# Kernel optimization log

Hardware: AMD Instinct MI355X
Metric: run time of the kernel (lower is better)

Reference implementation:

```python
import jax, jax.numpy as jnp
import numpy as np

B, S, H, I, G = 4, 2048, 2048, 8192, 128


def _onebit_quant(w, group_size):
    # Group-wise 1-bit (sign) quantization along the input dim with per-group
    # abs-mean scale, as in BitNet-style OneBitLinear.
    out_f, in_f = w.shape
    wg = w.reshape(out_f, in_f // group_size, group_size)
    scale = jnp.mean(jnp.abs(wg), axis=-1, keepdims=True)  # [out, n_groups, 1]
    wq = jnp.sign(wg) * scale
    return wq.reshape(out_f, in_f)


def setup_inputs() -> dict:
    key = jax.random.key(0)
    k1, k2, k3, k4 = jax.random.split(key, 4)
    return {
        "x": jax.random.normal(k1, (B, S, H), dtype=jnp.float32),
        "w_gate": jax.random.normal(k2, (I, H), dtype=jnp.float32) * 0.02,
        "w_up": jax.random.normal(k3, (I, H), dtype=jnp.float32) * 0.02,
        "w_down": jax.random.normal(k4, (H, I), dtype=jnp.float32) * 0.02,
        "group_size": G,
    }


def reference(x, w_gate, w_up, w_down, group_size):
    wg_q = _onebit_quant(w_gate, group_size)   # [I, H]
    wu_q = _onebit_quant(w_up, group_size)     # [I, H]
    wd_q = _onebit_quant(w_down, group_size)   # [H, I]
    gate = jnp.einsum('bsh,ih->bsi', x, wg_q)  # [B, S, I]
    up = jnp.einsum('bsh,ih->bsi', x, wu_q)    # [B, S, I]
    h = jax.nn.silu(gate) * up                 # [B, S, I]
    return jnp.einsum('bsi,hi->bsh', h, wd_q)  # [B, S, H]
```

## Files before the change

### kernel.cpp

```cpp
#include <hip/hip_runtime.h>
#include <hip/hip_bf16.h>
#include <cstdint>
#include <cstddef>

using bf16 = __hip_bfloat16;

typedef __attribute__((ext_vector_type(8))) short short8;
typedef __attribute__((ext_vector_type(16))) float f32x16;
typedef __attribute__((ext_vector_type(4))) unsigned short us4;

static constexpr int Bb = 4, Ss = 2048, Hh = 2048, Ii = 8192, Gg = 128;
static constexpr int Mm = Bb * Ss;

#define MEMFENCE() asm volatile("" ::: "memory")
#define BARRIER() do { MEMFENCE(); __builtin_amdgcn_s_barrier(); MEMFENCE(); } while (0)

__global__ void quant_onebit(const float* __restrict__ w, bf16* __restrict__ wq,
                             int ngroups) {
  int gid = blockIdx.x * 4 + (threadIdx.x >> 6);
  if (gid >= ngroups) return;
  int lane = threadIdx.x & 63;
  size_t base = (size_t)gid * Gg + (size_t)lane * 2;
  float2 v = *(const float2*)(w + base);
  float s = fabsf(v.x) + fabsf(v.y);
#pragma unroll
  for (int m = 32; m >= 1; m >>= 1) s += __shfl_xor(s, m);
  float scale = s * (1.0f / 128.0f);
  float q0 = (v.x > 0.f) ? scale : ((v.x < 0.f) ? -scale : 0.f);
  float q1 = (v.y > 0.f) ? scale : ((v.y < 0.f) ? -scale : 0.f);
  unsigned int p =
      (unsigned int)__builtin_bit_cast(unsigned short, __float2bfloat16(q0)) |
      ((unsigned int)__builtin_bit_cast(unsigned short, __float2bfloat16(q1)) << 16);
  *(unsigned int*)(wq + base) = p;
}

__global__ void cast_f32_bf16(const float* __restrict__ in, bf16* __restrict__ out,
                              size_t n4) {
  size_t i = (size_t)blockIdx.x * blockDim.x + threadIdx.x;
  if (i >= n4) return;
  float4 v = *(const float4*)(in + i * 4);
  us4 o;
  o.x = __builtin_bit_cast(unsigned short, __float2bfloat16(v.x));
  o.y = __builtin_bit_cast(unsigned short, __float2bfloat16(v.y));
  o.z = __builtin_bit_cast(unsigned short, __float2bfloat16(v.z));
  o.w = __builtin_bit_cast(unsigned short, __float2bfloat16(v.w));
  *(us4*)(out + i * 4) = o;
}

__device__ __forceinline__ void gload16(const bf16* g, char* l) {
  __builtin_amdgcn_global_load_lds(
      (const __attribute__((address_space(1))) void*)g,
      (__attribute__((address_space(3))) void*)l, 16, 0, 0);
}

__device__ __forceinline__ short8 lfrag(const char* part, int row, int s) {
  return *(const short8*)(part + row * 64 + (((s ^ (row >> 1)) & 3) << 4));
}

template <bool DUAL>
__global__ __launch_bounds__(512, 2)
void gemm_bt8(const bf16* __restrict__ A,
              const bf16* __restrict__ B0,
              const bf16* __restrict__ B1,
              bf16* __restrict__ OutBf,
              float* __restrict__ OutF,
              int M, int N, int K) {
  constexpr int BM = 256, BN = DUAL ? 128 : 256;
  extern __shared__ char smem[];

  const int tid = threadIdx.x;
  const int wid = tid >> 6;
  const int lane = tid & 63;
  const int wr = wid >> 2;
  const int wc = wid & 3;
  const int l31 = lane & 31;
  const int lh = lane >> 5;

  const int nbx = N / BN;
  const int nbm = M / BM;
  const int nwg = (int)gridDim.x;
  const int cpx = nwg >> 3;
  const int wg = (int)blockIdx.x;
  const int L = (wg & 7) * cpx + (wg >> 3);
  constexpr int CN = 8;
  const int chunk = L / (nbm * CN);
  const int within = L % (nbm * CN);
  const int m0 = (within / CN) * BM;
  const int n0 = (chunk * CN + (within % CN)) * BN;

  const int NT = K / 64;

  const int srow = tid >> 2;
  const int slog8 = (((tid & 3) ^ ((tid >> 3) & 3)) << 3);
  const bf16* pA0 = A + (size_t)(m0 + srow) * K + slog8;
  const bf16* pA1 = pA0 + (size_t)128 * K;
  const bf16* pB0 = B0 + (size_t)(n0 + srow) * K + slog8;
  const bf16* pB1 = DUAL ? (B1 + (size_t)(n0 + srow) * K + slog8)
                         : (pB0 + (size_t)128 * K);
  const int dA = wid * 1024;

  auto stageA = [&](int t, int p) {
    char* b = smem + (size_t)(t & 1) * 65536 + p * 32768;
    const int koff = t * 64 + p * 32;
    gload16(pA0 + koff, b + dA);
    gload16(pA1 + koff, b + 8192 + dA);
  };
  auto stageB = [&](int t, int p) {
    char* b = smem + (size_t)(t & 1) * 65536 + p * 32768 + 16384;
    const int koff = t * 64 + p * 32;
    gload16(pB0 + koff, b + dA);
    gload16(pB1 + koff, b + 8192 + dA);
  };

  const int aRowBase = wr * 128 + l31;
  const int bRow0 = (DUAL ? wc * 32 : wc * 64) + l31;
  const int bRow1 = DUAL ? bRow0 : (bRow0 + 32);

  const f32x16 vzero = {0.f};
  f32x16 acc0[4], acc1[4];
#pragma unroll
  for (int mf = 0; mf < 4; ++mf) { acc0[mf] = vzero; acc1[mf] = vzero; }

  stageA(0, 0); stageB(0, 0);
  stageA(0, 1); stageB(0, 1);

  short8 fa[4], fb0k[2], fb1k[2];

  for (int t = 0; t < NT; ++t) {
    const char* buf = smem + (size_t)(t & 1) * 65536;
#pragma unroll
    for (int p = 0; p < 2; ++p) {
      const char* Ap = buf + p * 32768;
      const char* Bp = Ap + 16384;
      const char* Bp1 = DUAL ? (Bp + 8192) : Bp;

      if (p == 0 || t + 1 < NT)
        asm volatile("s_waitcnt vmcnt(4)" ::: "memory");
      else
        asm volatile("s_waitcnt vmcnt(0)" ::: "memory");
      BARRIER();
#pragma unroll
      for (int ku = 0; ku < 2; ++ku) {
        fb0k[ku] = lfrag(Bp, bRow0, ku * 2 + lh);
        fb1k[ku] = lfrag(Bp1, bRow1, ku * 2 + lh);
      }
#pragma unroll
      for (int mf = 0; mf < 4; ++mf)
        fa[mf] = lfrag(Ap, aRowBase + mf * 32, lh);
      if (t + 1 < NT) stageA(t + 1, p);
      __builtin_amdgcn_s_setprio(1);
#pragma unroll
      for (int mf = 0; mf < 4; ++mf) {
        acc0[mf] = __builtin_amdgcn_mfma_f32_32x32x16_bf16(
            fa[mf], fb0k[0], acc0[mf], 0, 0, 0);
        acc1[mf] = __builtin_amdgcn_mfma_f32_32x32x16_bf16(
            fa[mf], fb1k[0], acc1[mf], 0, 0, 0);
      }
      __builtin_amdgcn_s_setprio(0);
      BARRIER();

#pragma unroll
      for (int mf = 0; mf < 4; ++mf)
        fa[mf] = lfrag(Ap, aRowBase + mf * 32, 2 + lh);
      if (t + 1 < NT) stageB(t + 1, p);
      __builtin_amdgcn_s_setprio(1);
#pragma unroll
      for (int mf = 0; mf < 4; ++mf) {
        acc0[mf] = __builtin_amdgcn_mfma_f32_32x32x16_bf16(
            fa[mf], fb0k[1], acc0[mf], 0, 0, 0);
        acc1[mf] = __builtin_amdgcn_mfma_f32_32x32x16_bf16(
            fa[mf], fb1k[1], acc1[mf], 0, 0, 0);
      }
      __builtin_amdgcn_s_setprio(0);
    }
  }

#pragma unroll
  for (int mf = 0; mf < 4; ++mf)
#pragma unroll
    for (int r = 0; r < 16; ++r) {
      const int row = m0 + wr * 128 + mf * 32 + (r & 3) + 8 * (r >> 2) + 4 * lh;
      if constexpr (DUAL) {
        const int col = n0 + wc * 32 + l31;
        float g = acc0[mf][r];
        float u = acc1[mf][r];
        OutBf[(size_t)row * N + col] =
            __float2bfloat16(g / (1.0f + expf(-g)) * u);
      } else {
        const int col = n0 + wc * 64 + l31;
        OutF[(size_t)row * N + col] = acc0[mf][r];
        OutF[(size_t)row * N + col + 32] = acc1[mf][r];
      }
    }
}

extern "C" void kernel_launch(void* const* d_in, const int* in_sizes, int n_in,
                              void* d_out, int out_size, void* d_ws, size_t ws_size,
                              hipStream_t stream) {
  const float* x = (const float*)d_in[0];
  const float* wg = (const float*)d_in[1];
  const float* wu = (const float*)d_in[2];
  const float* wd = (const float*)d_in[3];
  float* out = (float*)d_out;

  char* ws = (char*)d_ws;
  bf16* xq = (bf16*)(ws + 0);
  bf16* wgq = (bf16*)(ws + (size_t)33554432);
  bf16* wuq = (bf16*)(ws + (size_t)67108864);
  bf16* hbuf = (bf16*)(ws + (size_t)100663296);
  bf16* wdq = xq;

  auto* kDual = gemm_bt8<true>;
  auto* kSingle = gemm_bt8<false>;
  (void)hipFuncSetAttribute((const void*)kDual,
                            hipFuncAttributeMaxDynamicSharedMemorySize, 131072);
  (void)hipFuncSetAttribute((const void*)kSingle,
                            hipFuncAttributeMaxDynamicSharedMemorySize, 131072);

  const int ngW = (Ii * Hh) / Gg;
  quant_onebit<<<ngW / 4, 256, 0, stream>>>(wg, wgq, ngW);
  quant_onebit<<<ngW / 4, 256, 0, stream>>>(wu, wuq, ngW);

  const size_t n4 = (size_t)Mm * Hh / 4;
  cast_f32_bf16<<<(unsigned)((n4 + 255) / 256), 256, 0, stream>>>(x, xq, n4);

  kDual<<<(Mm / 256) * (Ii / 128), 512, 131072, stream>>>(
      xq, wgq, wuq, hbuf, nullptr, Mm, Ii, Hh);

  quant_onebit<<<ngW / 4, 256, 0, stream>>>(wd, wdq, ngW);

  kSingle<<<(Mm / 256) * (Hh / 256), 512, 131072, stream>>>(
      hbuf, wdq, nullptr, nullptr, out, Mm, Hh, Ii);
}
```

Baseline: 885.7 us.

## Restructure GEMM pipeline into six-slot k16 ring buffer with deeper prefetch

New measurement: 1.038 ms. 17.2% more time.

```diff
diff --git a/kernel.cpp b/kernel.cpp
--- a/kernel.cpp
+++ b/kernel.cpp
@@ -53,18 +53,14 @@
       (__attribute__((address_space(3))) void*)l, 16, 0, 0);
 }
 
-__device__ __forceinline__ short8 lfrag(const char* part, int row, int s) {
-  return *(const short8*)(part + row * 64 + (((s ^ (row >> 1)) & 3) << 4));
-}
-
 template <bool DUAL>
-__global__ __launch_bounds__(512, 2)
-void gemm_bt8(const bf16* __restrict__ A,
-              const bf16* __restrict__ B0,
-              const bf16* __restrict__ B1,
-              bf16* __restrict__ OutBf,
-              float* __restrict__ OutF,
-              int M, int N, int K) {
+__global__ __launch_bounds__(512, 1)
+void gemm32(const bf16* __restrict__ A,
+            const bf16* __restrict__ B0,
+            const bf16* __restrict__ B1,
+            bf16* __restrict__ OutBf,
+            float* __restrict__ OutF,
+            int M, int N, int K) {
   constexpr int BM = 256, BN = DUAL ? 128 : 256;
   extern __shared__ char smem[];
 
@@ -88,91 +84,89 @@
   const int m0 = (within / CN) * BM;
   const int n0 = (chunk * CN + (within % CN)) * BN;
 
-  const int NT = K / 64;
-
-  const int srow = tid >> 2;
-  const int slog8 = (((tid & 3) ^ ((tid >> 3) & 3)) << 3);
-  const bf16* pA0 = A + (size_t)(m0 + srow) * K + slog8;
-  const bf16* pA1 = pA0 + (size_t)128 * K;
-  const bf16* pB0 = B0 + (size_t)(n0 + srow) * K + slog8;
-  const bf16* pB1 = DUAL ? (B1 + (size_t)(n0 + srow) * K + slog8)
-                         : (pB0 + (size_t)128 * K);
+  const int NU = K >> 4;
+  const int NG = NU >> 1;
+
+  const int srow = tid >> 1;
+  const int scol = (((tid & 1) ^ ((tid >> 3) & 1)) << 3);
+  const bf16* pA = A + (size_t)(m0 + srow) * K + scol;
+  const bf16* pB;
+  if constexpr (DUAL)
+    pB = (srow < 128 ? B0 + (size_t)(n0 + srow) * K
+                     : B1 + (size_t)(n0 + srow - 128) * K) + scol;
+  else
+    pB = B0 + (size_t)(n0 + srow) * K + scol;
   const int dA = wid * 1024;
 
-  auto stageA = [&](int t, int p) {
-    char* b = smem + (size_t)(t & 1) * 65536 + p * 32768;
-    const int koff = t * 64 + p * 32;
-    gload16(pA0 + koff, b + dA);
-    gload16(pA1 + koff, b + 8192 + dA);
+  auto stage = [&](int v, int slot) {
+    char* b = smem + slot * 16384;
+    gload16(pA + v * 16, b + dA);
+    gload16(pB + v * 16, b + 8192 + dA);
   };
-  auto stageB = [&](int t, int p) {
-    char* b = smem + (size_t)(t & 1) * 65536 + p * 32768 + 16384;
-    const int koff = t * 64 + p * 32;
-    gload16(pB0 + koff, b + dA);
-    gload16(pB1 + koff, b + 8192 + dA);
+
+  auto lf = [&](const char* part, int row) -> short8 {
+    return *(const short8*)(part + row * 32 + (((lh ^ (row >> 2)) & 1) << 4));
   };
-
-  const int aRowBase = wr * 128 + l31;
-  const int bRow0 = (DUAL ? wc * 32 : wc * 64) + l31;
-  const int bRow1 = DUAL ? bRow0 : (bRow0 + 32);
 
   const f32x16 vzero = {0.f};
   f32x16 acc0[4], acc1[4];
 #pragma unroll
   for (int mf = 0; mf < 4; ++mf) { acc0[mf] = vzero; acc1[mf] = vzero; }
 
-  stageA(0, 0); stageB(0, 0);
-  stageA(0, 1); stageB(0, 1);
-
-  short8 fa[4], fb0k[2], fb1k[2];
-
-  for (int t = 0; t < NT; ++t) {
-    const char* buf = smem + (size_t)(t & 1) * 65536;
-#pragma unroll
-    for (int p = 0; p < 2; ++p) {
-      const char* Ap = buf + p * 32768;
-      const char* Bp = Ap + 16384;
-      const char* Bp1 = DUAL ? (Bp + 8192) : Bp;
-
-      if (p == 0 || t + 1 < NT)
-        asm volatile("s_waitcnt vmcnt(4)" ::: "memory");
-      else
-        asm volatile("s_waitcnt vmcnt(0)" ::: "memory");
-      BARRIER();
-#pragma unroll
-      for (int ku = 0; ku < 2; ++ku) {
-        fb0k[ku] = lfrag(Bp, bRow0, ku * 2 + lh);
-        fb1k[ku] = lfrag(Bp1, bRow1, ku * 2 + lh);
-      }
-#pragma unroll
-      for (int mf = 0; mf < 4; ++mf)
-        fa[mf] = lfrag(Ap, aRowBase + mf * 32, lh);
-      if (t + 1 < NT) stageA(t + 1, p);
-      __builtin_amdgcn_s_setprio(1);
-#pragma unroll
-      for (int mf = 0; mf < 4; ++mf) {
-        acc0[mf] = __builtin_amdgcn_mfma_f32_32x32x16_bf16(
-            fa[mf], fb0k[0], acc0[mf], 0, 0, 0);
-        acc1[mf] = __builtin_amdgcn_mfma_f32_32x32x16_bf16(
-            fa[mf], fb1k[0], acc1[mf], 0, 0, 0);
-      }
-      __builtin_amdgcn_s_setprio(0);
-      BARRIER();
-
-#pragma unroll
-      for (int mf = 0; mf < 4; ++mf)
-        fa[mf] = lfrag(Ap, aRowBase + mf * 32, 2 + lh);
-      if (t + 1 < NT) stageB(t + 1, p);
-      __builtin_amdgcn_s_setprio(1);
-#pragma unroll
-      for (int mf = 0; mf < 4; ++mf) {
-        acc0[mf] = __builtin_amdgcn_mfma_f32_32x32x16_bf16(
-            fa[mf], fb0k[1], acc0[mf], 0, 0, 0);
-        acc1[mf] = __builtin_amdgcn_mfma_f32_32x32x16_bf16(
-            fa[mf], fb1k[1], acc1[mf], 0, 0, 0);
-      }
-      __builtin_amdgcn_s_setprio(0);
-    }
+  stage(0, 0); stage(1, 1); stage(2, 2); stage(3, 3);
+
+  short8 fa[4], fb0, fb1;
+  int sb = 0;
+
+  for (int g = 0; g < NG; ++g) {
+    if (g + 1 < NG) asm volatile("s_waitcnt vmcnt(4)" ::: "memory");
+    else            asm volatile("s_waitcnt vmcnt(0)" ::: "memory");
+    BARRIER();
+
+    const int u0 = 2 * g;
+    const char* Au0 = smem + sb * 16384;
+    const char* Au1 = Au0 + 16384;
+    int sp = sb + 4; if (sp >= 6) sp -= 6;
+
+#pragma unroll
+    for (int mf = 0; mf < 4; ++mf)
+      fa[mf] = lf(Au0, wr * 128 + mf * 32 + l31);
+    if constexpr (DUAL) {
+      fb0 = lf(Au0 + 8192, wc * 32 + l31);
+      fb1 = lf(Au0 + 8192, 128 + wc * 32 + l31);
+    } else {
+      fb0 = lf(Au0 + 8192, wc * 64 + l31);
+      fb1 = lf(Au0 + 8192, wc * 64 + 32 + l31);
+    }
+    if (u0 + 4 < NU) stage(u0 + 4, sp);
+    __builtin_amdgcn_s_setprio(1);
+#pragma unroll
+    for (int mf = 0; mf < 4; ++mf) {
+      acc0[mf] = __builtin_amdgcn_mfma_f32_32x32x16_bf16(fa[mf], fb0, acc0[mf], 0, 0, 0);
+      acc1[mf] = __builtin_amdgcn_mfma_f32_32x32x16_bf16(fa[mf], fb1, acc1[mf], 0, 0, 0);
+    }
+    __builtin_amdgcn_s_setprio(0);
+
+#pragma unroll
+    for (int mf = 0; mf < 4; ++mf)
+      fa[mf] = lf(Au1, wr * 128 + mf * 32 + l31);
+    if constexpr (DUAL) {
+      fb0 = lf(Au1 + 8192, wc * 32 + l31);
+      fb1 = lf(Au1 + 8192, 128 + wc * 32 + l31);
+    } else {
+      fb0 = lf(Au1 + 8192, wc * 64 + l31);
+      fb1 = lf(Au1 + 8192, wc * 64 + 32 + l31);
+    }
+    if (u0 + 5 < NU) stage(u0 + 5, sp + 1);
+    __builtin_amdgcn_s_setprio(1);
+#pragma unroll
+    for (int mf = 0; mf < 4; ++mf) {
+      acc0[mf] = __builtin_amdgcn_mfma_f32_32x32x16_bf16(fa[mf], fb0, acc0[mf], 0, 0, 0);
+      acc1[mf] = __builtin_amdgcn_mfma_f32_32x32x16_bf16(fa[mf], fb1, acc1[mf], 0, 0, 0);
+    }
+    __builtin_amdgcn_s_setprio(0);
+
+    sb += 2; if (sb >= 6) sb = 0;
   }
 
 #pragma unroll
@@ -210,12 +204,12 @@
   bf16* hbuf = (bf16*)(ws + (size_t)100663296);
   bf16* wdq = xq;
 
-  auto* kDual = gemm_bt8<true>;
-  auto* kSingle = gemm_bt8<false>;
+  auto* kDual = gemm32<true>;
+  auto* kSingle = gemm32<false>;
   (void)hipFuncSetAttribute((const void*)kDual,
-                            hipFuncAttributeMaxDynamicSharedMemorySize, 131072);
+                            hipFuncAttributeMaxDynamicSharedMemorySize, 98304);
   (void)hipFuncSetAttribute((const void*)kSingle,
-                            hipFuncAttributeMaxDynamicSharedMemorySize, 131072);
+                            hipFuncAttributeMaxDynamicSharedMemorySize, 98304);
 
   const int ngW = (Ii * Hh) / Gg;
   quant_onebit<<<ngW / 4, 256, 0, stream>>>(wg, wgq, ngW);
@@ -224,11 +218,11 @@
   const size_t n4 = (size_t)Mm * Hh / 4;
   cast_f32_bf16<<<(unsigned)((n4 + 255) / 256), 256, 0, stream>>>(x, xq, n4);
 
-  kDual<<<(Mm / 256) * (Ii / 128), 512, 131072, stream>>>(
+  kDual<<<(Mm / 256) * (Ii / 128), 512, 98304, stream>>>(
       xq, wgq, wuq, hbuf, nullptr, Mm, Ii, Hh);
 
   quant_onebit<<<ngW / 4, 256, 0, stream>>>(wd, wdq, ngW);
 
-  kSingle<<<(Mm / 256) * (Hh / 256), 512, 131072, stream>>>(
+  kSingle<<<(Mm / 256) * (Hh / 256), 512, 98304, stream>>>(
       hbuf, wdq, nullptr, nullptr, out, Mm, Hh, Ii);
 }
```

## Re-tile LDS staging into 32-row by 16-k blocks matching MFMA fragments

Applied to the files above, without the earlier changes.

After: 877.3 us. About the same (-1.0%).

```diff
diff --git a/kernel.cpp b/kernel.cpp
--- a/kernel.cpp
+++ b/kernel.cpp
@@ -53,18 +53,14 @@
       (__attribute__((address_space(3))) void*)l, 16, 0, 0);
 }
 
-__device__ __forceinline__ short8 lfrag(const char* part, int row, int s) {
-  return *(const short8*)(part + row * 64 + (((s ^ (row >> 1)) & 3) << 4));
-}
-
 template <bool DUAL>
 __global__ __launch_bounds__(512, 2)
-void gemm_bt8(const bf16* __restrict__ A,
-              const bf16* __restrict__ B0,
-              const bf16* __restrict__ B1,
-              bf16* __restrict__ OutBf,
-              float* __restrict__ OutF,
-              int M, int N, int K) {
+void gemm32(const bf16* __restrict__ A,
+            const bf16* __restrict__ B0,
+            const bf16* __restrict__ B1,
+            bf16* __restrict__ OutBf,
+            float* __restrict__ OutF,
+            int M, int N, int K) {
   constexpr int BM = 256, BN = DUAL ? 128 : 256;
   extern __shared__ char smem[];
 
@@ -74,7 +70,10 @@
   const int wr = wid >> 2;
   const int wc = wid & 3;
   const int l31 = lane & 31;
+  const int lrow = lane & 15;
+  const int q = lane >> 4;
   const int lh = lane >> 5;
+  const int rdOff = 64 * lrow + (((q ^ (lrow >> 1)) & 3) << 4);
 
   const int nbx = N / BN;
   const int nbm = M / BM;
@@ -90,31 +89,34 @@
 
   const int NT = K / 64;
 
-  const int srow = tid >> 2;
-  const int slog8 = (((tid & 3) ^ ((tid >> 3) & 3)) << 3);
-  const bf16* pA0 = A + (size_t)(m0 + srow) * K + slog8;
-  const bf16* pA1 = pA0 + (size_t)128 * K;
-  const bf16* pB0 = B0 + (size_t)(n0 + srow) * K + slog8;
-  const bf16* pB1 = DUAL ? (B1 + (size_t)(n0 + srow) * K + slog8)
-                         : (pB0 + (size_t)128 * K);
+  const int lrs = (tid >> 2) & 15;
+  const int cq = (tid & 3) ^ ((lrs >> 1) & 3);
+  const int srow = (wid << 5) + ((cq & 1) << 4) + lrs;
+  const int skoff = (cq >> 1) << 3;
+  const bf16* pA = A + (size_t)(m0 + srow) * K + skoff;
+  const bf16* pB;
+  if constexpr (DUAL)
+    pB = (srow < 128 ? B0 + (size_t)(n0 + srow) * K
+                     : B1 + (size_t)(n0 + srow - 128) * K) + skoff;
+  else
+    pB = B0 + (size_t)(n0 + srow) * K + skoff;
   const int dA = wid * 1024;
 
   auto stageA = [&](int t, int p) {
     char* b = smem + (size_t)(t & 1) * 65536 + p * 32768;
     const int koff = t * 64 + p * 32;
-    gload16(pA0 + koff, b + dA);
-    gload16(pA1 + koff, b + 8192 + dA);
+    gload16(pA + koff, b + dA);
+    gload16(pA + koff + 16, b + 8192 + dA);
   };
   auto stageB = [&](int t, int p) {
     char* b = smem + (size_t)(t & 1) * 65536 + p * 32768 + 16384;
     const int koff = t * 64 + p * 32;
-    gload16(pB0 + koff, b + dA);
-    gload16(pB1 + koff, b + 8192 + dA);
+    gload16(pB + koff, b + dA);
+    gload16(pB + koff + 16, b + 8192 + dA);
   };
 
-  const int aRowBase = wr * 128 + l31;
-  const int bRow0 = (DUAL ? wc * 32 : wc * 64) + l31;
-  const int bRow1 = DUAL ? bRow0 : (bRow0 + 32);
+  const int gB0 = DUAL ? wc : (2 * wc);
+  const int gB1 = DUAL ? (4 + wc) : (2 * wc + 1);
 
   const f32x16 vzero = {0.f};
   f32x16 acc0[4], acc1[4];
@@ -124,15 +126,13 @@
   stageA(0, 0); stageB(0, 0);
   stageA(0, 1); stageB(0, 1);
 
-  short8 fa[4], fb0k[2], fb1k[2];
+  short8 fa[4], fb0, fb1;
 
   for (int t = 0; t < NT; ++t) {
     const char* buf = smem + (size_t)(t & 1) * 65536;
 #pragma unroll
     for (int p = 0; p < 2; ++p) {
-      const char* Ap = buf + p * 32768;
-      const char* Bp = Ap + 16384;
-      const char* Bp1 = DUAL ? (Bp + 8192) : Bp;
+      const char* Sp = buf + p * 32768;
 
       if (p == 0 || t + 1 < NT)
         asm volatile("s_waitcnt vmcnt(4)" ::: "memory");
@@ -140,36 +140,31 @@
         asm volatile("s_waitcnt vmcnt(0)" ::: "memory");
       BARRIER();
 #pragma unroll
-      for (int ku = 0; ku < 2; ++ku) {
-        fb0k[ku] = lfrag(Bp, bRow0, ku * 2 + lh);
-        fb1k[ku] = lfrag(Bp1, bRow1, ku * 2 + lh);
-      }
-#pragma unroll
       for (int mf = 0; mf < 4; ++mf)
-        fa[mf] = lfrag(Ap, aRowBase + mf * 32, lh);
+        fa[mf] = *(const short8*)(Sp + (wr * 4 + mf) * 1024 + rdOff);
+      fb0 = *(const short8*)(Sp + 16384 + gB0 * 1024 + rdOff);
+      fb1 = *(const short8*)(Sp + 16384 + gB1 * 1024 + rdOff);
       if (t + 1 < NT) stageA(t + 1, p);
       __builtin_amdgcn_s_setprio(1);
 #pragma unroll
       for (int mf = 0; mf < 4; ++mf) {
-        acc0[mf] = __builtin_amdgcn_mfma_f32_32x32x16_bf16(
-            fa[mf], fb0k[0], acc0[mf], 0, 0, 0);
-        acc1[mf] = __builtin_amdgcn_mfma_f32_32x32x16_bf16(
-            fa[mf], fb1k[0], acc1[mf], 0, 0, 0);
+        acc0[mf] = __builtin_amdgcn_mfma_f32_32x32x16_bf16(fa[mf], fb0, acc0[mf], 0, 0, 0);
+        acc1[mf] = __builtin_amdgcn_mfma_f32_32x32x16_bf16(fa[mf], fb1, acc1[mf], 0, 0, 0);
       }
       __builtin_amdgcn_s_setprio(0);
       BARRIER();
 
 #pragma unroll
       for (int mf = 0; mf < 4; ++mf)
-        fa[mf] = lfrag(Ap, aRowBase + mf * 32, 2 + lh);
+        fa[mf] = *(const short8*)(Sp + 8192 + (wr * 4 + mf) * 1024 + rdOff);
+      fb0 = *(const short8*)(Sp + 8192 + 16384 + gB0 * 1024 + rdOff);
+      fb1 = *(const short8*)(Sp + 8192 + 16384 + gB1 * 1024 + rdOff);
       if (t + 1 < NT) stageB(t + 1, p);
       __builtin_amdgcn_s_setprio(1);
 #pragma unroll
       for (int mf = 0; mf < 4; ++mf) {
-        acc0[mf] = __builtin_amdgcn_mfma_f32_32x32x16_bf16(
-            fa[mf], fb0k[1], acc0[mf], 0, 0, 0);
-        acc1[mf] = __builtin_amdgcn_mfma_f32_32x32x16_bf16(
-            fa[mf], fb1k[1], acc1[mf], 0, 0, 0);
+        acc0[mf] = __builtin_amdgcn_mfma_f32_32x32x16_bf16(fa[mf], fb0, acc0[mf], 0, 0, 0);
+        acc1[mf] = __builtin_amdgcn_mfma_f32_32x32x16_bf16(fa[mf], fb1, acc1[mf], 0, 0, 0);
       }
       __builtin_amdgcn_s_setprio(0);
     }
@@ -210,8 +205,8 @@
   bf16* hbuf = (bf16*)(ws + (size_t)100663296);
   bf16* wdq = xq;
 
-  auto* kDual = gemm_bt8<true>;
-  auto* kSingle = gemm_bt8<false>;
+  auto* kDual = gemm32<true>;
+  auto* kSingle = gemm32<false>;
   (void)hipFuncSetAttribute((const void*)kDual,
                             hipFuncAttributeMaxDynamicSharedMemorySize, 131072);
   (void)hipFuncSetAttribute((const void*)kSingle,
```
